# Performance work log

Hardware: AMD Instinct MI355X
Metric: run time of the kernel (lower is better)

The kernel has to match this reference:

```python
import jax, jax.numpy as jnp
import numpy as np

NUM_HEADS = 16

def _stablemax3_s(x):
    # 3rd-order Taylor approx of exp(x), Eq 38
    pos = 1.0 + x * (1.0 + 0.5 * x * (1.0 + x / 3.0))
    neg = 1.0 / (1.0 - x * (1.0 - 0.5 * x * (1.0 - x / 3.0)))
    return jnp.where(x >= 0, pos, neg)

def stablemax3(logits, axis=-1):
    logits = logits - jnp.max(logits, axis=axis, keepdims=True)
    s = _stablemax3_s(logits)
    return s / jnp.sum(s, axis=axis, keepdims=True)

def setup_inputs() -> dict:
    key = jax.random.key(0)
    k1, k2, k3 = jax.random.split(key, 3)
    B, S, D = 2, 2048, 1024
    x = jax.random.normal(k1, (B, S, D), dtype=jnp.float32)
    w_qkv = jax.random.normal(k2, (3 * D, D), dtype=jnp.float32) * 0.02
    w_out = jax.random.normal(k3, (D, D), dtype=jnp.float32) * 0.02
    b_out = jnp.zeros((D,), dtype=jnp.float32)
    return {"x": x, "w_qkv": w_qkv, "w_out": w_out, "b_out": b_out}

def reference(x, w_qkv, w_out, b_out):
    B, S, D = x.shape
    H = NUM_HEADS
    hd = D // H
    scale = hd ** (-0.5)
    qkv = x @ w_qkv.T                                  # [B, S, 3D]
    qkv = qkv.reshape(B, S, 3, H, hd)
    qkv = jnp.transpose(qkv, (2, 0, 3, 1, 4))          # [3, B, H, S, hd]
    q, k, v = qkv[0], qkv[1], qkv[2]                   # pos(.) is identity here
    attn = jnp.einsum('bhsd,bhtd->bhst', q, k) * scale # [B, H, S, S]
    attn = stablemax3(attn, axis=-1)
    out = jnp.einsum('bhst,bhtd->bhsd', attn, v)       # [B, H, S, hd]
    out = jnp.transpose(out, (0, 2, 1, 3)).reshape(B, S, D)
    return out @ w_out.T + b_out
```

## Files before the change

kernel.cpp:

```cpp
#include <hip/hip_runtime.h>

typedef _Float16 half8 __attribute__((ext_vector_type(8)));
typedef _Float16 half4 __attribute__((ext_vector_type(4)));
typedef float floatx4 __attribute__((ext_vector_type(4)));

__global__ __launch_bounds__(256) void gemm_qkv(const float* __restrict__ X,
                                                const float* __restrict__ W,
                                                _Float16* __restrict__ qh,
                                                _Float16* __restrict__ kh,
                                                _Float16* __restrict__ vth) {
    const int K = 1024;
    __shared__ _Float16 SH[128 * 40 * 2];
    _Float16* As = SH;
    _Float16* Bs = SH + 128 * 40;
    const int t = threadIdx.x;
    const int lane = t & 63, w = t >> 6;
    const int l15 = lane & 15, quad = lane >> 4;
    const int wm = w >> 1, wn = w & 1;
    const int m0 = blockIdx.y * 128, n0 = blockIdx.x * 128;

    floatx4 acc[4][4];
    const floatx4 zf = {0.f, 0.f, 0.f, 0.f};
#pragma unroll
    for (int i = 0; i < 4; ++i)
#pragma unroll
        for (int j = 0; j < 4; ++j) acc[i][j] = zf;

    for (int kt = 0; kt < K; kt += 32) {
        __syncthreads();
#pragma unroll
        for (int it = 0; it < 4; ++it) {
            int cc = it * 256 + t;
            int row = cc >> 3, c4 = cc & 7;
            floatx4 xv = *(const floatx4*)&X[(size_t)(m0 + row) * K + kt + c4 * 4];
            floatx4 wv = *(const floatx4*)&W[(size_t)(n0 + row) * K + kt + c4 * 4];
            half4 xh, wh;
#pragma unroll
            for (int j = 0; j < 4; ++j) { xh[j] = (_Float16)xv[j]; wh[j] = (_Float16)wv[j]; }
            *(half4*)&As[row * 40 + c4 * 4] = xh;
            *(half4*)&Bs[row * 40 + c4 * 4] = wh;
        }
        __syncthreads();
        half8 af[4], bfr[4];
#pragma unroll
        for (int i = 0; i < 4; ++i)
            af[i] = *(const half8*)&As[(wm * 64 + i * 16 + l15) * 40 + quad * 8];
#pragma unroll
        for (int i = 0; i < 4; ++i)
            bfr[i] = *(const half8*)&Bs[(wn * 64 + i * 16 + l15) * 40 + quad * 8];
#pragma unroll
        for (int mi = 0; mi < 4; ++mi)
#pragma unroll
            for (int ni = 0; ni < 4; ++ni)
                acc[mi][ni] = __builtin_amdgcn_mfma_f32_16x16x32_f16(af[mi], bfr[ni],
                                                                     acc[mi][ni], 0, 0, 0);
    }

    const int b = m0 >> 11, s0 = m0 & 2047;
#pragma unroll
    for (int hf = 0; hf < 2; ++hf) {
        __syncthreads();
        if (wn == hf) {
#pragma unroll
            for (int mi = 0; mi < 4; ++mi)
#pragma unroll
                for (int ni = 0; ni < 4; ++ni)
#pragma unroll
                    for (int r = 0; r < 4; ++r)
                        SH[(wm * 64 + mi * 16 + quad * 4 + r) * 68 + ni * 16 + l15] =
                            (_Float16)acc[mi][ni][r];
        }
        __syncthreads();
        const int cbase = n0 + hf * 64;
        if (n0 < 2048) {
            const int hh = (cbase & 1023) >> 6;
            _Float16* dst = (n0 < 1024 ? qh : kh) + (size_t)((b << 4) | hh) * 131072;
#pragma unroll
            for (int it = 0; it < 4; ++it) {
                int cc = it * 256 + t;
                int r = cc >> 3, c8 = cc & 7;
                half4 lo = *(const half4*)&SH[r * 68 + c8 * 8];
                half4 hi = *(const half4*)&SH[r * 68 + c8 * 8 + 4];
                half8 v;
#pragma unroll
                for (int j = 0; j < 4; ++j) { v[j] = lo[j]; v[j + 4] = hi[j]; }
                *(half8*)&dst[(size_t)(s0 + r) * 64 + c8 * 8] = v;
            }
        } else {
            const int hh = (cbase - 2048) >> 6;
            _Float16* dst = vth + (size_t)((b << 4) | hh) * 131072;
#pragma unroll
            for (int it = 0; it < 4; ++it) {
                int cc = it * 256 + t;
                int d = cc >> 4, s8 = cc & 15;
                half8 v;
#pragma unroll
                for (int j = 0; j < 8; ++j) v[j] = SH[(s8 * 8 + j) * 68 + d];
                *(half8*)&dst[(size_t)d * 2048 + s0 + s8 * 8] = v;
            }
        }
    }
}

__global__ __launch_bounds__(256) void gemm_out(const _Float16* __restrict__ A,
                                                const float* __restrict__ W,
                                                float* __restrict__ C,
                                                const float* __restrict__ bias) {
    const int K = 1024, N = 1024;
    __shared__ _Float16 As[64 * 40];
    __shared__ _Float16 Bs[128 * 40];
    const int t = threadIdx.x;
    const int lane = t & 63, w = t >> 6;
    const int l15 = lane & 15, quad = lane >> 4;
    const int wm = w >> 1, wn = w & 1;
    const int m0 = blockIdx.y * 64, n0 = blockIdx.x * 128;

    floatx4 acc[2][4];
    const floatx4 zf = {0.f, 0.f, 0.f, 0.f};
#pragma unroll
    for (int i = 0; i < 2; ++i)
#pragma unroll
        for (int j = 0; j < 4; ++j) acc[i][j] = zf;

    for (int kt = 0; kt < K; kt += 32) {
        __syncthreads();
        {
            int row = t >> 2, kc = t & 3;
            *(half8*)&As[row * 40 + kc * 8] =
                *(const half8*)&A[(size_t)(m0 + row) * K + kt + kc * 8];
        }
#pragma unroll
        for (int it = 0; it < 4; ++it) {
            int cc = it * 256 + t;
            int row = cc >> 3, c4 = cc & 7;
            floatx4 wv = *(const floatx4*)&W[(size_t)(n0 + row) * K + kt + c4 * 4];
            half4 wh;
#pragma unroll
            for (int j = 0; j < 4; ++j) wh[j] = (_Float16)wv[j];
            *(half4*)&Bs[row * 40 + c4 * 4] = wh;
        }
        __syncthreads();
        half8 af[2], bfr[4];
#pragma unroll
        for (int i = 0; i < 2; ++i)
            af[i] = *(const half8*)&As[(wm * 32 + i * 16 + l15) * 40 + quad * 8];
#pragma unroll
        for (int i = 0; i < 4; ++i)
            bfr[i] = *(const half8*)&Bs[(wn * 64 + i * 16 + l15) * 40 + quad * 8];
#pragma unroll
        for (int mi = 0; mi < 2; ++mi)
#pragma unroll
            for (int ni = 0; ni < 4; ++ni)
                acc[mi][ni] = __builtin_amdgcn_mfma_f32_16x16x32_f16(af[mi], bfr[ni],
                                                                     acc[mi][ni], 0, 0, 0);
    }

#pragma unroll
    for (int mi = 0; mi < 2; ++mi) {
#pragma unroll
        for (int ni = 0; ni < 4; ++ni) {
            int col = n0 + wn * 64 + ni * 16 + l15;
            float bv = bias[col];
#pragma unroll
            for (int r = 0; r < 4; ++r) {
                int row = m0 + wm * 32 + mi * 16 + quad * 4 + r;
                C[(size_t)row * N + col] = acc[mi][ni][r] + bv;
            }
        }
    }
}

__device__ inline float s3pos(float a) {
    float h = fmaf(a, 0.16666667f, 0.5f);
    h = fmaf(a, h, 1.0f);
    return fmaf(a, h, 1.0f);
}

__global__ __launch_bounds__(256) void attn_kernel(const _Float16* __restrict__ qh,
                                                   const _Float16* __restrict__ kh,
                                                   const _Float16* __restrict__ vth,
                                                   _Float16* __restrict__ out) {
    __shared__ _Float16 SM[2 * 64 * 72];
    _Float16* Ks = SM;
    _Float16* VTs = SM + 64 * 72;

    const int t = threadIdx.x;
    const int lane = t & 63, w = t >> 6;
    const int l15 = lane & 15, quad = lane >> 4;
    const int q0 = blockIdx.x * 128;
    const int bh = blockIdx.y;
    const int b = bh >> 4, h = bh & 15;

    const _Float16* Qp = qh + (size_t)bh * 131072 + q0 * 64;
    const _Float16* Kp = kh + (size_t)bh * 131072;
    const _Float16* VTp = vth + (size_t)bh * 131072;

    const floatx4 zf = {0.f, 0.f, 0.f, 0.f};

    half8 qf[2][2];
#pragma unroll
    for (int nh = 0; nh < 2; ++nh)
#pragma unroll
        for (int kk = 0; kk < 2; ++kk)
            qf[nh][kk] = *(const half8*)&Qp[(w * 32 + nh * 16 + l15) * 64 + kk * 32 + quad * 8];

    float rmax[2] = {-1.0e30f, -1.0e30f};

    for (int kt = 0; kt < 2048; kt += 64) {
        __syncthreads();
#pragma unroll
        for (int it = 0; it < 2; ++it) {
            int cc = it * 256 + t;
            int r = cc >> 3, c8 = cc & 7;
            *(half8*)&Ks[r * 72 + c8 * 8] = *(const half8*)&Kp[kt * 64 + cc * 8];
        }
        __syncthreads();
        floatx4 sa[4][2];
#pragma unroll
        for (int T = 0; T < 4; ++T) { sa[T][0] = zf; sa[T][1] = zf; }
#pragma unroll
        for (int kk = 0; kk < 2; ++kk) {
            half8 kf[4];
#pragma unroll
            for (int T = 0; T < 4; ++T)
                kf[T] = *(const half8*)&Ks[(T * 16 + l15) * 72 + kk * 32 + quad * 8];
#pragma unroll
            for (int T = 0; T < 4; ++T)
#pragma unroll
                for (int nh = 0; nh < 2; ++nh)
                    sa[T][nh] = __builtin_amdgcn_mfma_f32_16x16x32_f16(kf[T], qf[nh][kk],
                                                                      sa[T][nh], 0, 0, 0);
        }
#pragma unroll
        for (int T = 0; T < 4; ++T)
#pragma unroll
            for (int nh = 0; nh < 2; ++nh)
#pragma unroll
                for (int r = 0; r < 4; ++r)
                    rmax[nh] = fmaxf(rmax[nh], sa[T][nh][r]);
    }
#pragma unroll
    for (int nh = 0; nh < 2; ++nh) {
        rmax[nh] = fmaxf(rmax[nh], __shfl_xor(rmax[nh], 16, 64));
        rmax[nh] = fmaxf(rmax[nh], __shfl_xor(rmax[nh], 32, 64));
    }
    const float xm[2] = {-0.125f * rmax[0], -0.125f * rmax[1]};

    float rsum[2] = {0.f, 0.f};
    floatx4 oacc[4][2];
#pragma unroll
    for (int i = 0; i < 4; ++i) { oacc[i][0] = zf; oacc[i][1] = zf; }

    for (int kt = 0; kt < 2048; kt += 64) {
        __syncthreads();
#pragma unroll
        for (int it = 0; it < 2; ++it) {
            int cc = it * 256 + t;
            int r = cc >> 3, c8 = cc & 7;
            *(half8*)&Ks[r * 72 + c8 * 8] = *(const half8*)&Kp[kt * 64 + cc * 8];
            *(half8*)&VTs[r * 72 + c8 * 8] =
                *(const half8*)&VTp[(size_t)r * 2048 + kt + c8 * 8];
        }
        __syncthreads();
        floatx4 sa[4][2];
#pragma unroll
        for (int T = 0; T < 4; ++T) { sa[T][0] = zf; sa[T][1] = zf; }
#pragma unroll
        for (int kk = 0; kk < 2; ++kk) {
            half8 kf[4];
#pragma unroll
            for (int T = 0; T < 4; ++T)
                kf[T] = *(const half8*)&Ks[(T * 16 + l15) * 72 + kk * 32 + quad * 8];
#pragma unroll
            for (int T = 0; T < 4; ++T)
#pragma unroll
                for (int nh = 0; nh < 2; ++nh)
                    sa[T][nh] = __builtin_amdgcn_mfma_f32_16x16x32_f16(kf[T], qf[nh][kk],
                                                                      sa[T][nh], 0, 0, 0);
        }
        float p[2][4][4];
#pragma unroll
        for (int nh = 0; nh < 2; ++nh)
#pragma unroll
            for (int T = 0; T < 4; ++T)
#pragma unroll
                for (int r = 0; r < 4; ++r) {
                    float x = fmaf(sa[T][nh][r], 0.125f, xm[nh]);
                    float pv = __builtin_amdgcn_rcpf(s3pos(fabsf(x)));
                    p[nh][T][r] = pv;
                    rsum[nh] += pv;
                }
#pragma unroll
        for (int c = 0; c < 2; ++c) {
            half8 vf[4];
#pragma unroll
            for (int di = 0; di < 4; ++di) {
                half4 lo = *(const half4*)&VTs[(di * 16 + l15) * 72 + c * 32 + 4 * quad];
                half4 hi = *(const half4*)&VTs[(di * 16 + l15) * 72 + c * 32 + 16 + 4 * quad];
                half8 vv;
#pragma unroll
                for (int j = 0; j < 4; ++j) { vv[j] = lo[j]; vv[j + 4] = hi[j]; }
                vf[di] = vv;
            }
#pragma unroll
            for (int nh = 0; nh < 2; ++nh) {
                half8 pb;
#pragma unroll
                for (int j = 0; j < 8; ++j)
                    pb[j] = (_Float16)p[nh][2 * c + (j >> 2)][j & 3];
#pragma unroll
                for (int di = 0; di < 4; ++di)
                    oacc[di][nh] = __builtin_amdgcn_mfma_f32_16x16x32_f16(vf[di], pb,
                                                                         oacc[di][nh], 0, 0, 0);
            }
        }
    }

#pragma unroll
    for (int nh = 0; nh < 2; ++nh) {
        rsum[nh] += __shfl_xor(rsum[nh], 16, 64);
        rsum[nh] += __shfl_xor(rsum[nh], 32, 64);
    }
    const float inv[2] = {1.0f / rsum[0], 1.0f / rsum[1]};

    __syncthreads();
    _Float16* Os = SM;
#pragma unroll
    for (int di = 0; di < 4; ++di) {
#pragma unroll
        for (int nh = 0; nh < 2; ++nh) {
            half4 hv;
#pragma unroll
            for (int r = 0; r < 4; ++r) hv[r] = (_Float16)(oacc[di][nh][r] * inv[nh]);
            *(half4*)&Os[(w * 32 + nh * 16 + l15) * 72 + di * 16 + quad * 4] = hv;
        }
    }
    __syncthreads();
    _Float16* Op = out + (size_t)(b * 2048 + q0) * 1024 + h * 64;
#pragma unroll
    for (int it = 0; it < 4; ++it) {
        int cc = it * 256 + t;
        int r = cc >> 3, c8 = cc & 7;
        *(half8*)&Op[(size_t)r * 1024 + c8 * 8] = *(const half8*)&Os[r * 72 + c8 * 8];
    }
}

extern "C" void kernel_launch(void* const* d_in, const int* in_sizes, int n_in,
                              void* d_out, int out_size, void* d_ws, size_t ws_size,
                              hipStream_t stream) {
    const float* x_f = (const float*)d_in[0];
    const float* wqkv_f = (const float*)d_in[1];
    const float* wout_f = (const float*)d_in[2];
    const float* bias_f = (const float*)d_in[3];

    char* ws = (char*)d_ws;
    _Float16* qh = (_Float16*)(ws);
    _Float16* kh = (_Float16*)(ws + 8388608);
    _Float16* vth = (_Float16*)(ws + 16777216);
    _Float16* aoh = (_Float16*)(ws + 25165824);

    gemm_qkv<<<dim3(24, 32), 256, 0, stream>>>(x_f, wqkv_f, qh, kh, vth);
    attn_kernel<<<dim3(16, 32), 256, 0, stream>>>(qh, kh, vth, aoh);
    gemm_out<<<dim3(8, 64), 256, 0, stream>>>(aoh, wout_f, (float*)d_out, bias_f);
}
```

Baseline: 234.8 us.

## Pre-convert inputs to fp16 and load GEMM tiles directly into LDS

Adds separate conversion kernels that turn x, w_qkv and w_out from fp32 to fp16 in workspace. Both GEMMs then stage tiles with global_load_lds (16-byte direct-to-LDS loads) instead of loading fp32, converting in registers and storing to LDS. This halves the global bytes read inside the GEMM loops and removes per-thread conversion work. In exchange it adds three extra launches plus a full read/write pass over the inputs, and drops the LDS row padding (stride 32 instead of 40), which may bring bank conflicts on the fragment reads.

```diff
diff --git a/kernel.cpp b/kernel.cpp
--- a/kernel.cpp
+++ b/kernel.cpp
@@ -4,15 +4,32 @@
 typedef _Float16 half4 __attribute__((ext_vector_type(4)));
 typedef float floatx4 __attribute__((ext_vector_type(4)));
 
-__global__ __launch_bounds__(256) void gemm_qkv(const float* __restrict__ X,
-                                                const float* __restrict__ W,
+__device__ __forceinline__ void gl_lds16(const _Float16* g, _Float16* l) {
+    __builtin_amdgcn_global_load_lds(
+        (const __attribute__((address_space(1))) void*)g,
+        (__attribute__((address_space(3))) void*)l, 16, 0, 0);
+}
+
+__global__ __launch_bounds__(256) void cvt_f32_f16(const floatx4* __restrict__ in,
+                                                   half4* __restrict__ out, int n4) {
+    int i = blockIdx.x * 256 + threadIdx.x;
+    if (i >= n4) return;
+    floatx4 v = in[i];
+    half4 h;
+#pragma unroll
+    for (int j = 0; j < 4; ++j) h[j] = (_Float16)v[j];
+    out[i] = h;
+}
+
+__global__ __launch_bounds__(256) void gemm_qkv(const _Float16* __restrict__ A,
+                                                const _Float16* __restrict__ B,
                                                 _Float16* __restrict__ qh,
                                                 _Float16* __restrict__ kh,
                                                 _Float16* __restrict__ vth) {
     const int K = 1024;
-    __shared__ _Float16 SH[128 * 40 * 2];
+    __shared__ _Float16 SH[128 * 68];
     _Float16* As = SH;
-    _Float16* Bs = SH + 128 * 40;
+    _Float16* Bs = SH + 4096;
     const int t = threadIdx.x;
     const int lane = t & 63, w = t >> 6;
     const int l15 = lane & 15, quad = lane >> 4;
@@ -29,25 +46,20 @@
     for (int kt = 0; kt < K; kt += 32) {
         __syncthreads();
 #pragma unroll
-        for (int it = 0; it < 4; ++it) {
+        for (int it = 0; it < 2; ++it) {
             int cc = it * 256 + t;
-            int row = cc >> 3, c4 = cc & 7;
-            floatx4 xv = *(const floatx4*)&X[(size_t)(m0 + row) * K + kt + c4 * 4];
-            floatx4 wv = *(const floatx4*)&W[(size_t)(n0 + row) * K + kt + c4 * 4];
-            half4 xh, wh;
-#pragma unroll
-            for (int j = 0; j < 4; ++j) { xh[j] = (_Float16)xv[j]; wh[j] = (_Float16)wv[j]; }
-            *(half4*)&As[row * 40 + c4 * 4] = xh;
-            *(half4*)&Bs[row * 40 + c4 * 4] = wh;
+            int row = cc >> 2, kc = cc & 3;
+            gl_lds16(&A[(size_t)(m0 + row) * K + kt + kc * 8], &As[cc * 8]);
+            gl_lds16(&B[(size_t)(n0 + row) * K + kt + kc * 8], &Bs[cc * 8]);
         }
         __syncthreads();
         half8 af[4], bfr[4];
 #pragma unroll
         for (int i = 0; i < 4; ++i)
-            af[i] = *(const half8*)&As[(wm * 64 + i * 16 + l15) * 40 + quad * 8];
+            af[i] = *(const half8*)&As[(wm * 64 + i * 16 + l15) * 32 + quad * 8];
 #pragma unroll
         for (int i = 0; i < 4; ++i)
-            bfr[i] = *(const half8*)&Bs[(wn * 64 + i * 16 + l15) * 40 + quad * 8];
+            bfr[i] = *(const half8*)&Bs[(wn * 64 + i * 16 + l15) * 32 + quad * 8];
 #pragma unroll
         for (int mi = 0; mi < 4; ++mi)
 #pragma unroll
@@ -103,12 +115,13 @@
 }
 
 __global__ __launch_bounds__(256) void gemm_out(const _Float16* __restrict__ A,
-                                                const float* __restrict__ W,
+                                                const _Float16* __restrict__ B,
                                                 float* __restrict__ C,
                                                 const float* __restrict__ bias) {
     const int K = 1024, N = 1024;
-    __shared__ _Float16 As[64 * 40];
-    __shared__ _Float16 Bs[128 * 40];
+    __shared__ _Float16 SH[6144];
+    _Float16* As = SH;
+    _Float16* Bs = SH + 2048;
     const int t = threadIdx.x;
     const int lane = t & 63, w = t >> 6;
     const int l15 = lane & 15, quad = lane >> 4;
@@ -126,27 +139,22 @@
         __syncthreads();
         {
             int row = t >> 2, kc = t & 3;
-            *(half8*)&As[row * 40 + kc * 8] =
-                *(const half8*)&A[(size_t)(m0 + row) * K + kt + kc * 8];
-        }
-#pragma unroll
-        for (int it = 0; it < 4; ++it) {
+            gl_lds16(&A[(size_t)(m0 + row) * K + kt + kc * 8], &As[t * 8]);
+        }
+#pragma unroll
+        for (int it = 0; it < 2; ++it) {
             int cc = it * 256 + t;
-            int row = cc >> 3, c4 = cc & 7;
-            floatx4 wv = *(const floatx4*)&W[(size_t)(n0 + row) * K + kt + c4 * 4];
-            half4 wh;
-#pragma unroll
-            for (int j = 0; j < 4; ++j) wh[j] = (_Float16)wv[j];
-            *(half4*)&Bs[row * 40 + c4 * 4] = wh;
+            int row = cc >> 2, kc = cc & 3;
+            gl_lds16(&B[(size_t)(n0 + row) * K + kt + kc * 8], &Bs[cc * 8]);
         }
         __syncthreads();
         half8 af[2], bfr[4];
 #pragma unroll
         for (int i = 0; i < 2; ++i)
-            af[i] = *(const half8*)&As[(wm * 32 + i * 16 + l15) * 40 + quad * 8];
+            af[i] = *(const half8*)&As[(wm * 32 + i * 16 + l15) * 32 + quad * 8];
 #pragma unroll
         for (int i = 0; i < 4; ++i)
-            bfr[i] = *(const half8*)&Bs[(wn * 64 + i * 16 + l15) * 40 + quad * 8];
+            bfr[i] = *(const half8*)&Bs[(wn * 64 + i * 16 + l15) * 32 + quad * 8];
 #pragma unroll
         for (int mi = 0; mi < 2; ++mi)
 #pragma unroll
@@ -354,12 +362,18 @@
     const float* bias_f = (const float*)d_in[3];
 
     char* ws = (char*)d_ws;
-    _Float16* qh = (_Float16*)(ws);
-    _Float16* kh = (_Float16*)(ws + 8388608);
-    _Float16* vth = (_Float16*)(ws + 16777216);
-    _Float16* aoh = (_Float16*)(ws + 25165824);
-
-    gemm_qkv<<<dim3(24, 32), 256, 0, stream>>>(x_f, wqkv_f, qh, kh, vth);
+    _Float16* xh = (_Float16*)(ws);
+    _Float16* aoh = xh;
+    _Float16* wqh = (_Float16*)(ws + 8388608);
+    _Float16* woh = wqh;
+    _Float16* qh = (_Float16*)(ws + 14680064);
+    _Float16* kh = (_Float16*)(ws + 23068672);
+    _Float16* vth = (_Float16*)(ws + 31457280);
+
+    cvt_f32_f16<<<4096, 256, 0, stream>>>((const floatx4*)x_f, (half4*)xh, 1048576);
+    cvt_f32_f16<<<3072, 256, 0, stream>>>((const floatx4*)wqkv_f, (half4*)wqh, 786432);
+    gemm_qkv<<<dim3(24, 32), 256, 0, stream>>>(xh, wqh, qh, kh, vth);
+    cvt_f32_f16<<<1024, 256, 0, stream>>>((const floatx4*)wout_f, (half4*)woh, 262144);
     attn_kernel<<<dim3(16, 32), 256, 0, stream>>>(qh, kh, vth, aoh);
-    gemm_out<<<dim3(8, 64), 256, 0, stream>>>(aoh, wout_f, (float*)d_out, bias_f);
-}
+    gemm_out<<<dim3(8, 64), 256, 0, stream>>>(aoh, woh, (float*)d_out, bias_f);
+}
```

Result: faster. 218.3 us (median of 2 runs) (-7.0%).
